# Kernel optimization log

Hardware: AMD Instinct MI355X
Metric: run time of the kernel (lower is better)

Reference implementation:

```python
import jax, jax.numpy as jnp
import numpy as np

N = 100000   # nodes
D = 128      # embedding dim
E = 1600000  # edges (avg in-degree 16)
EPS = 1e-15
MAX_TANH_ARG = 1.0 - 1e-7  # keep arctanh finite


def _logmap0(x):
    # Poincare-ball logmap at the origin: artanh(||x||) * x / ||x||
    norm = jnp.linalg.norm(x, axis=-1, keepdims=True)
    safe = jnp.maximum(norm, EPS)
    return jnp.arctanh(jnp.clip(norm, 0.0, MAX_TANH_ARG)) * x / safe


def _expmap0(v):
    # Poincare-ball expmap at the origin: tanh(||v||) * v / ||v||
    norm = jnp.linalg.norm(v, axis=-1, keepdims=True)
    safe = jnp.maximum(norm, EPS)
    return jnp.tanh(norm) * v / safe


def setup_inputs() -> dict:
    key = jax.random.key(0)
    k1, k2, k3, k4, k5 = jax.random.split(key, 5)
    # small norms keep points strictly inside the unit ball
    x = jax.random.normal(k1, (N, D), dtype=jnp.float32) * 0.01
    src = jax.random.randint(k2, (E,), 0, N)
    dst = jax.random.randint(k3, (E,), 0, N)
    W = jax.random.normal(k4, (D, D), dtype=jnp.float32) * (1.0 / np.sqrt(D))
    b = jax.random.normal(k5, (D,), dtype=jnp.float32) * 0.01
    return {"x": x, "W": W, "b": b, "src": src, "dst": dst}


def reference(x, W, b, src, dst):
    # logmap to tangent space at origin
    tangent_x = _logmap0(x)
    # linear layer (nn.Linear: x @ W^T + b)
    h = tangent_x @ W.T + b  # [N, D]
    # copy_u + mean aggregation over in-neighbors (DGL update_all)
    msg_sum = jax.ops.segment_sum(h[src], dst, num_segments=N)      # [N, D]
    deg = jax.ops.segment_sum(jnp.ones((E,), h.dtype), dst, num_segments=N)
    neigh = msg_sum / jnp.maximum(deg, 1.0)[:, None]  # zero-degree nodes -> 0 (DGL mean)
    # expmap back onto the Poincare ball
    return _expmap0(neigh)
```

## Files before the change

### kernel.cpp

```cpp
#include <hip/hip_runtime.h>
#include <hip/hip_fp16.h>
#include <math.h>

constexpr int D = 128;
constexpr int BSH = 9;
constexpr int BNODES = 1 << BSH;
constexpr int NBLK = 256;

typedef __attribute__((ext_vector_type(8))) short bf16x8;
typedef __attribute__((ext_vector_type(4))) float f32x4;

__device__ inline short f2bf(float f) {
    unsigned u = __builtin_bit_cast(unsigned, f);
    u = (u + 0x7FFFu + ((u >> 16) & 1u)) >> 16;
    return (short)u;
}

__global__ __launch_bounds__(256) void part_hist_kernel(
    const int* __restrict__ dst, int* __restrict__ blkhist,
    int nEdges, int NB)
{
    __shared__ int hist[256];
    int t = threadIdx.x;
    hist[t] = 0;
    __syncthreads();

    int per = (nEdges + gridDim.x - 1) / gridDim.x;
    int i0 = blockIdx.x * per;
    int i1 = min(nEdges, i0 + per);
    for (int i = i0 + t; i < i1; i += 256)
        atomicAdd(&hist[dst[i] >> BSH], 1);
    __syncthreads();
    if (t < NB) blkhist[t * NBLK + blockIdx.x] = hist[t];
}

__global__ __launch_bounds__(256) void part_scan1_kernel(
    int* __restrict__ blkhist, int* __restrict__ btot)
{
    __shared__ int s[256];
    int b = blockIdx.x;
    int t = threadIdx.x;
    int v = blkhist[b * NBLK + t];
    s[t] = v;
    __syncthreads();
    for (int off = 1; off < 256; off <<= 1) {
        int xv = (t >= off) ? s[t - off] : 0;
        __syncthreads();
        if (t >= off) s[t] += xv;
        __syncthreads();
    }
    blkhist[b * NBLK + t] = s[t] - v;
    if (t == 255) btot[b] = s[255];
}

__global__ __launch_bounds__(256) void part_scan2_kernel(
    const int* __restrict__ btot, int* __restrict__ bbase,
    int NB, int nEdges)
{
    __shared__ int s[256];
    int t = threadIdx.x;
    int v = (t < NB) ? btot[t] : 0;
    s[t] = v;
    __syncthreads();
    for (int off = 1; off < 256; off <<= 1) {
        int xv = (t >= off) ? s[t - off] : 0;
        __syncthreads();
        if (t >= off) s[t] += xv;
        __syncthreads();
    }
    if (t < NB) bbase[t] = s[t] - v;
    if (t == 0) bbase[NB] = nEdges;
}

__global__ __launch_bounds__(256) void part_scatter_kernel(
    const int* __restrict__ src, const int* __restrict__ dst,
    const int* __restrict__ blkhist, const int* __restrict__ bbase,
    unsigned* __restrict__ part, int nEdges, int NB)
{
    __shared__ int cur[256];
    int t = threadIdx.x;
    cur[t] = (t < NB) ? (blkhist[t * NBLK + blockIdx.x] + bbase[t]) : 0;
    __syncthreads();

    int per = (nEdges + gridDim.x - 1) / gridDim.x;
    int i0 = blockIdx.x * per;
    int i1 = min(nEdges, i0 + per);
    for (int i = i0 + t; i < i1; i += 256) {
        int d = dst[i];
        int b = d >> BSH;
        int p = atomicAdd(&cur[b], 1);
        part[p] = (unsigned)src[i] | ((unsigned)(d & (BNODES - 1)) << 17);
    }
}

__global__ __launch_bounds__(256) void bucket_csr_kernel(
    const unsigned* __restrict__ part, const int* __restrict__ bbase,
    int* __restrict__ rowptr, float* __restrict__ degf,
    int* __restrict__ csr_src, int nNodes, int NB, int nEdges)
{
    __shared__ int cnt[BNODES];
    __shared__ int excl[BNODES];
    __shared__ int cur[BNODES];
    __shared__ int s[256];

    int b = blockIdx.x;
    int t = threadIdx.x;
    int bb = bbase[b], be = bbase[b + 1];

    cnt[t] = 0; cnt[t + 256] = 0;
    cur[t] = 0; cur[t + 256] = 0;
    __syncthreads();

    for (int i = bb + t; i < be; i += 256)
        atomicAdd(&cnt[part[i] >> 17], 1);
    __syncthreads();

    int a0 = cnt[2 * t], a1 = cnt[2 * t + 1];
    s[t] = a0 + a1;
    __syncthreads();
    for (int off = 1; off < 256; off <<= 1) {
        int xv = (t >= off) ? s[t - off] : 0;
        __syncthreads();
        if (t >= off) s[t] += xv;
        __syncthreads();
    }
    int pbase = (t > 0) ? s[t - 1] : 0;
    excl[2 * t]     = pbase;
    excl[2 * t + 1] = pbase + a0;
    __syncthreads();

    int node0 = b << BSH;
#pragma unroll
    for (int q = 0; q < 2; ++q) {
        int j = t + q * 256;
        int d = node0 + j;
        if (d < nNodes) {
            rowptr[d] = bb + excl[j];
            degf[d]   = (float)cnt[j];
        }
    }
    if (b == NB - 1 && t == 0) rowptr[nNodes] = nEdges;

    for (int i = bb + t; i < be; i += 256) {
        unsigned v = part[i];
        int dloc = v >> 17;
        int p = bb + excl[dloc] + atomicAdd(&cur[dloc], 1);
        csr_src[p] = (int)(v & 0x1FFFFu);
    }
}

__global__ __launch_bounds__(256) void hist_win_kernel(
    const int* __restrict__ dst, int* __restrict__ count,
    int nEdges, int winSize)
{
    int pass    = blockIdx.x & 7;
    int slice   = blockIdx.x >> 3;
    int nSlices = gridDim.x >> 3;
    int lo = pass * winSize;
    int hi = lo + winSize;

    int stride = nSlices * blockDim.x;
    for (int i = slice * blockDim.x + threadIdx.x; i < nEdges; i += stride) {
        int d = dst[i];
        if (d >= lo && d < hi) atomicAdd(&count[d], 1);
    }
}

__global__ __launch_bounds__(256) void scan_block_kernel(
    const int* __restrict__ count, int* __restrict__ rowptr,
    int* __restrict__ blksums, int n)
{
    __shared__ int sums[256];
    int t = threadIdx.x;
    int base = blockIdx.x * 1024 + t * 4;
    int v[4];
    int s = 0;
#pragma unroll
    for (int j = 0; j < 4; ++j) { v[j] = (base + j < n) ? count[base + j] : 0; s += v[j]; }
    sums[t] = s;
    __syncthreads();
    for (int off = 1; off < 256; off <<= 1) {
        int xv = (t >= off) ? sums[t - off] : 0;
        __syncthreads();
        if (t >= off) sums[t] += xv;
        __syncthreads();
    }
    int run = (t > 0) ? sums[t - 1] : 0;
#pragma unroll
    for (int j = 0; j < 4; ++j) { if (base + j < n) rowptr[base + j] = run; run += v[j]; }
    if (t == 255) blksums[blockIdx.x] = sums[255];
}

__global__ __launch_bounds__(256) void scan_totals_kernel(
    int* __restrict__ blksums, int* __restrict__ rowptr,
    int numBlocks, int n, int E)
{
    __shared__ int s[256];
    int t = threadIdx.x;
    s[t] = (t < numBlocks) ? blksums[t] : 0;
    __syncthreads();
    for (int off = 1; off < 256; off <<= 1) {
        int xv = (t >= off) ? s[t - off] : 0;
        __syncthreads();
        if (t >= off) s[t] += xv;
        __syncthreads();
    }
    if (t < numBlocks) blksums[t] = (t > 0) ? s[t - 1] : 0;
    if (t == 0) rowptr[n] = E;
}

__global__ __launch_bounds__(256) void add_offsets_kernel(
    int* __restrict__ rowptr, const int* __restrict__ blksums, int n)
{
    int i = blockIdx.x * 256 + threadIdx.x;
    if (i < n) rowptr[i] += blksums[i >> 10];
}

__global__ __launch_bounds__(256) void fill_win_kernel(
    const int* __restrict__ src, const int* __restrict__ dst,
    const int* __restrict__ rowptr, int* __restrict__ count,
    int* __restrict__ csr_src, int nEdges, int winSize)
{
    int pass    = blockIdx.x & 7;
    int slice   = blockIdx.x >> 3;
    int nSlices = gridDim.x >> 3;
    int lo = pass * winSize;
    int hi = lo + winSize;

    int stride = nSlices * blockDim.x;
    for (int i = slice * blockDim.x + threadIdx.x; i < nEdges; i += stride) {
        int d = dst[i];
        if (d >= lo && d < hi) {
            int pos = rowptr[d] + atomicSub(&count[d], 1) - 1;
            csr_src[pos] = src[i];
        }
    }
}

__global__ __launch_bounds__(256) void deg_from_rowptr_kernel(
    const int* __restrict__ rowptr, float* __restrict__ degf, int n)
{
    int i = blockIdx.x * 256 + threadIdx.x;
    if (i < n) degf[i] = (float)(rowptr[i + 1] - rowptr[i]);
}

__global__ __launch_bounds__(256) void tangent_kernel(
    const float* __restrict__ x, __half* __restrict__ th, int nNodes)
{
    int n    = (blockIdx.x * 256 + threadIdx.x) >> 6;
    int lane = threadIdx.x & 63;
    if (n >= nNodes) return;
    float2 xv = *reinterpret_cast<const float2*>(x + (size_t)n * D + lane * 2);
    float ss = xv.x * xv.x + xv.y * xv.y;
    ss += __shfl_xor(ss, 1);
    ss += __shfl_xor(ss, 2);
    ss += __shfl_xor(ss, 4);
    ss += __shfl_xor(ss, 8);
    ss += __shfl_xor(ss, 16);
    ss += __shfl_xor(ss, 32);
    float norm = sqrtf(ss);
    float ncl  = fminf(norm, 1.0f - 1e-7f);
    float at   = 0.5f * logf((1.0f + ncl) / (1.0f - ncl));
    float sc   = at / fmaxf(norm, 1e-15f);
    __half2 h = __float22half2_rn(make_float2(xv.x * sc, xv.y * sc));
    *(reinterpret_cast<__half2*>(th + (size_t)n * D) + lane) = h;
}

__global__ __launch_bounds__(256) void scale_kernel(
    const float* __restrict__ x, float* __restrict__ scale, int nNodes)
{
    int node = (blockIdx.x * 256 + threadIdx.x) >> 6;
    int lane = threadIdx.x & 63;
    if (node >= nNodes) return;
    float2 xv = *reinterpret_cast<const float2*>(x + (size_t)node * D + lane * 2);
    float ss = xv.x * xv.x + xv.y * xv.y;
    ss += __shfl_xor(ss, 1);
    ss += __shfl_xor(ss, 2);
    ss += __shfl_xor(ss, 4);
    ss += __shfl_xor(ss, 8);
    ss += __shfl_xor(ss, 16);
    ss += __shfl_xor(ss, 32);
    if (lane == 0) {
        float norm = sqrtf(ss);
        float ncl  = fminf(norm, 1.0f - 1e-7f);
        float at   = 0.5f * logf((1.0f + ncl) / (1.0f - ncl));
        scale[node] = at / fmaxf(norm, 1e-15f);
    }
}

__global__ __launch_bounds__(256) void gather_h16b_kernel(
    const __half* __restrict__ th,
    const int* __restrict__ csr_src, const int* __restrict__ rowptr,
    short* __restrict__ msgb, int nNodes)
{
    int n    = blockIdx.x * 4 + (threadIdx.x >> 6);
    int lane = threadIdx.x & 63;
    if (n >= nNodes) return;
    int grp = lane >> 4;
    int sl  = lane & 15;

    int beg = rowptr[n];
    int cnt = rowptr[n + 1] - beg;

    __half2 z = __float2half2_rn(0.0f);
    __half2 acc0[4] = {z, z, z, z};
    __half2 acc1[4] = {z, z, z, z};

    int k = grp;
    for (; k + 12 < cnt; k += 16) {
        int s0 = csr_src[beg + k];
        int s1 = csr_src[beg + k + 4];
        int s2 = csr_src[beg + k + 8];
        int s3 = csr_src[beg + k + 12];
        float4 r0 = *reinterpret_cast<const float4*>(th + (size_t)s0 * D + sl * 8);
        float4 r1 = *reinterpret_cast<const float4*>(th + (size_t)s1 * D + sl * 8);
        float4 r2 = *reinterpret_cast<const float4*>(th + (size_t)s2 * D + sl * 8);
        float4 r3 = *reinterpret_cast<const float4*>(th + (size_t)s3 * D + sl * 8);
        const __half2* h0 = reinterpret_cast<const __half2*>(&r0);
        const __half2* h1 = reinterpret_cast<const __half2*>(&r1);
        const __half2* h2 = reinterpret_cast<const __half2*>(&r2);
        const __half2* h3 = reinterpret_cast<const __half2*>(&r3);
#pragma unroll
        for (int j = 0; j < 4; ++j) {
            acc0[j] = __hadd2(acc0[j], h0[j]);
            acc1[j] = __hadd2(acc1[j], h1[j]);
            acc0[j] = __hadd2(acc0[j], h2[j]);
            acc1[j] = __hadd2(acc1[j], h3[j]);
        }
    }
    for (; k < cnt; k += 4) {
        int s0 = csr_src[beg + k];
        float4 r0 = *reinterpret_cast<const float4*>(th + (size_t)s0 * D + sl * 8);
        const __half2* h0 = reinterpret_cast<const __half2*>(&r0);
#pragma unroll
        for (int j = 0; j < 4; ++j) acc0[j] = __hadd2(acc0[j], h0[j]);
    }
#pragma unroll
    for (int j = 0; j < 4; ++j) {
        acc0[j] = __hadd2(acc0[j], acc1[j]);
        float f16 = __shfl_xor(__builtin_bit_cast(float, acc0[j]), 16);
        acc0[j] = __hadd2(acc0[j], __builtin_bit_cast(__half2, f16));
        float f32v = __shfl_xor(__builtin_bit_cast(float, acc0[j]), 32);
        acc0[j] = __hadd2(acc0[j], __builtin_bit_cast(__half2, f32v));
    }
    if (grp == 0) {
        short s8[8];
#pragma unroll
        for (int j = 0; j < 4; ++j) {
            float2 f = __half22float2(acc0[j]);
            s8[2 * j]     = f2bf(f.x);
            s8[2 * j + 1] = f2bf(f.y);
        }
        *reinterpret_cast<float4*>(msgb + (size_t)n * D + sl * 8) =
            *reinterpret_cast<float4*>(s8);
    }
}

__global__ __launch_bounds__(256) void gather_h16_kernel(
    const __half* __restrict__ th,
    const int* __restrict__ csr_src, const int* __restrict__ rowptr,
    float* __restrict__ msg, int nNodes)
{
    int n    = blockIdx.x * 4 + (threadIdx.x >> 6);
    int lane = threadIdx.x & 63;
    if (n >= nNodes) return;
    int grp = lane >> 4;
    int sl  = lane & 15;

    int beg = rowptr[n];
    int cnt = rowptr[n + 1] - beg;

    __half2 z = __float2half2_rn(0.0f);
    __half2 acc0[4] = {z, z, z, z};
    __half2 acc1[4] = {z, z, z, z};

    int k = grp;
    for (; k + 12 < cnt; k += 16) {
        int s0 = csr_src[beg + k];
        int s1 = csr_src[beg + k + 4];
        int s2 = csr_src[beg + k + 8];
        int s3 = csr_src[beg + k + 12];
        float4 r0 = *reinterpret_cast<const float4*>(th + (size_t)s0 * D + sl * 8);
        float4 r1 = *reinterpret_cast<const float4*>(th + (size_t)s1 * D + sl * 8);
        float4 r2 = *reinterpret_cast<const float4*>(th + (size_t)s2 * D + sl * 8);
        float4 r3 = *reinterpret_cast<const float4*>(th + (size_t)s3 * D + sl * 8);
        const __half2* h0 = reinterpret_cast<const __half2*>(&r0);
        const __half2* h1 = reinterpret_cast<const __half2*>(&r1);
        const __half2* h2 = reinterpret_cast<const __half2*>(&r2);
        const __half2* h3 = reinterpret_cast<const __half2*>(&r3);
#pragma unroll
        for (int j = 0; j < 4; ++j) {
            acc0[j] = __hadd2(acc0[j], h0[j]);
            acc1[j] = __hadd2(acc1[j], h1[j]);
            acc0[j] = __hadd2(acc0[j], h2[j]);
            acc1[j] = __hadd2(acc1[j], h3[j]);
        }
    }
    for (; k < cnt; k += 4) {
        int s0 = csr_src[beg + k];
        float4 r0 = *reinterpret_cast<const float4*>(th + (size_t)s0 * D + sl * 8);
        const __half2* h0 = reinterpret_cast<const __half2*>(&r0);
#pragma unroll
        for (int j = 0; j < 4; ++j) acc0[j] = __hadd2(acc0[j], h0[j]);
    }
#pragma unroll
    for (int j = 0; j < 4; ++j) {
        acc0[j] = __hadd2(acc0[j], acc1[j]);
        float f16 = __shfl_xor(__builtin_bit_cast(float, acc0[j]), 16);
        acc0[j] = __hadd2(acc0[j], __builtin_bit_cast(__half2, f16));
        float f32v = __shfl_xor(__builtin_bit_cast(float, acc0[j]), 32);
        acc0[j] = __hadd2(acc0[j], __builtin_bit_cast(__half2, f32v));
    }
    if (grp == 0) {
        float2 f0 = __half22float2(acc0[0]);
        float2 f1 = __half22float2(acc0[1]);
        float2 f2 = __half22float2(acc0[2]);
        float2 f3 = __half22float2(acc0[3]);
        float4 o0 = make_float4(f0.x, f0.y, f1.x, f1.y);
        float4 o1 = make_float4(f2.x, f2.y, f3.x, f3.y);
        *reinterpret_cast<float4*>(msg + (size_t)n * D + sl * 8)     = o0;
        *reinterpret_cast<float4*>(msg + (size_t)n * D + sl * 8 + 4) = o1;
    }
}

__global__ __launch_bounds__(256) void gather_kernel(
    const float* __restrict__ x, const float* __restrict__ scale,
    const int* __restrict__ csr_src, const int* __restrict__ rowptr,
    float* __restrict__ msg, float* __restrict__ degf, int nNodes)
{
    int n    = blockIdx.x * 4 + (threadIdx.x >> 6);
    int lane = threadIdx.x & 63;
    if (n >= nNodes) return;

    int beg = rowptr[n], end = rowptr[n + 1];
    float2 acc0 = make_float2(0.0f, 0.0f);
    float2 acc1 = make_float2(0.0f, 0.0f);
    int e = beg;
    for (; e + 3 < end; e += 4) {
        int s0 = csr_src[e],     s1 = csr_src[e + 1];
        int s2 = csr_src[e + 2], s3 = csr_src[e + 3];
        float sc0 = scale[s0], sc1 = scale[s1];
        float sc2 = scale[s2], sc3 = scale[s3];
        float2 a = *reinterpret_cast<const float2*>(x + (size_t)s0 * D + lane * 2);
        float2 b = *reinterpret_cast<const float2*>(x + (size_t)s1 * D + lane * 2);
        float2 c = *reinterpret_cast<const float2*>(x + (size_t)s2 * D + lane * 2);
        float2 d = *reinterpret_cast<const float2*>(x + (size_t)s3 * D + lane * 2);
        acc0.x += sc0 * a.x;  acc0.y += sc0 * a.y;
        acc1.x += sc1 * b.x;  acc1.y += sc1 * b.y;
        acc0.x += sc2 * c.x;  acc0.y += sc2 * c.y;
        acc1.x += sc3 * d.x;  acc1.y += sc3 * d.y;
    }
    for (; e < end; ++e) {
        int s0 = csr_src[e];
        float sc0 = scale[s0];
        float2 a = *reinterpret_cast<const float2*>(x + (size_t)s0 * D + lane * 2);
        acc0.x += sc0 * a.x;  acc0.y += sc0 * a.y;
    }
    acc0.x += acc1.x;  acc0.y += acc1.y;
    *reinterpret_cast<float2*>(msg + (size_t)n * D + lane * 2) = acc0;
    if (lane == 0) degf[n] = (float)(end - beg);
}

__global__ __launch_bounds__(256) void edge_scatter_kernel(
    const float* __restrict__ x,
    const int* __restrict__ src,
    const int* __restrict__ dst,
    float* __restrict__ msg,
    float* __restrict__ deg,
    int nEdges)
{
    long long t = (long long)blockIdx.x * blockDim.x + threadIdx.x;
    int edge = (int)(t >> 5);
    int lane = (int)(t & 31);
    if (edge >= nEdges) return;

    int s = src[edge];
    int d = dst[edge];

    const float4 xv = *reinterpret_cast<const float4*>(x + (size_t)s * D + lane * 4);
    float ss = xv.x * xv.x + xv.y * xv.y + xv.z * xv.z + xv.w * xv.w;
    ss += __shfl_xor(ss, 1);
    ss += __shfl_xor(ss, 2);
    ss += __shfl_xor(ss, 4);
    ss += __shfl_xor(ss, 8);
    ss += __shfl_xor(ss, 16);

    float norm = sqrtf(ss);
    float ncl  = fminf(norm, 1.0f - 1e-7f);
    float at   = 0.5f * logf((1.0f + ncl) / (1.0f - ncl));
    float scale = at / fmaxf(norm, 1e-15f);

    float* mrow = msg + (size_t)d * D + lane * 4;
    unsafeAtomicAdd(mrow + 0, xv.x * scale);
    unsafeAtomicAdd(mrow + 1, xv.y * scale);
    unsafeAtomicAdd(mrow + 2, xv.z * scale);
    unsafeAtomicAdd(mrow + 3, xv.w * scale);
    if (lane == 0) unsafeAtomicAdd(deg + d, 1.0f);
}

__global__ __launch_bounds__(256) void gemm_mfma_b_kernel(
    const short* __restrict__ msgb, const float* __restrict__ deg,
    const float* __restrict__ W, const float* __restrict__ bias,
    float* __restrict__ out, int nNodes)
{
    __shared__ short sW[128][136];

    const int t = threadIdx.x;

#pragma unroll
    for (int p = 0; p < 16; ++p) {
        int chunk = p * 256 + t;
        int row = chunk >> 5;
        int c4  = (chunk & 31) * 4;
        float4 v = *reinterpret_cast<const float4*>(W + row * 128 + c4);
        short4 s;
        s.x = f2bf(v.x); s.y = f2bf(v.y); s.z = f2bf(v.z); s.w = f2bf(v.w);
        *reinterpret_cast<short4*>(&sW[row][c4]) = s;
    }
    __syncthreads();

    const int wave = t >> 6;
    const int lane = t & 63;
    const int l15  = lane & 15;
    const int lhi  = lane >> 4;
    const int m0   = blockIdx.x * 64 + wave * 16;

    int arow = m0 + l15;
    if (arow >= nNodes) arow = nNodes - 1;
    const short* ap = msgb + (size_t)arow * D + lhi * 8;
    bf16x8 a[4];
#pragma unroll
    for (int kc = 0; kc < 4; ++kc)
        a[kc] = *reinterpret_cast<const bf16x8*>(ap + kc * 32);

    f32x4 acc[8];
#pragma unroll
    for (int ct = 0; ct < 8; ++ct) acc[ct] = (f32x4){0.f, 0.f, 0.f, 0.f};

#pragma unroll
    for (int ct = 0; ct < 8; ++ct) {
#pragma unroll
        for (int kc = 0; kc < 4; ++kc) {
            bf16x8 bfrag = *reinterpret_cast<const bf16x8*>(
                &sW[ct * 16 + l15][kc * 32 + lhi * 8]);
            acc[ct] = __builtin_amdgcn_mfma_f32_16x16x32_bf16(a[kc], bfrag, acc[ct], 0, 0, 0);
        }
    }

    float bv[8];
#pragma unroll
    for (int ct = 0; ct < 8; ++ct) bv[ct] = bias[ct * 16 + l15];

#pragma unroll
    for (int r = 0; r < 4; ++r) {
        int row = m0 + lhi * 4 + r;
        int rc  = row < nNodes ? row : nNodes - 1;
        float dg  = deg[rc];
        float inv = 1.0f / fmaxf(dg, 1.0f);
        float v[8];
        float ss = 0.0f;
#pragma unroll
        for (int ct = 0; ct < 8; ++ct) {
            v[ct] = acc[ct][r] * inv + bv[ct];
            ss += v[ct] * v[ct];
        }
        ss += __shfl_xor(ss, 1);
        ss += __shfl_xor(ss, 2);
        ss += __shfl_xor(ss, 4);
        ss += __shfl_xor(ss, 8);
        float norm = sqrtf(ss);
        float sc = (dg > 0.0f) ? (tanhf(norm) / fmaxf(norm, 1e-15f)) : 0.0f;
        if (row < nNodes) {
#pragma unroll
            for (int ct = 0; ct < 8; ++ct)
                out[(size_t)row * D + ct * 16 + l15] = v[ct] * sc;
        }
    }
}

__global__ __launch_bounds__(256) void gemm_mfma_kernel(
    const float* msg, const float* __restrict__ deg,
    const float* __restrict__ W, const float* __restrict__ bias,
    float* out, int nNodes)
{
    __shared__ short sW[128][136];

    const int t = threadIdx.x;

#pragma unroll
    for (int p = 0; p < 16; ++p) {
        int chunk = p * 256 + t;
        int row = chunk >> 5;
        int c4  = (chunk & 31) * 4;
        float4 v = *reinterpret_cast<const float4*>(W + row * 128 + c4);
        short4 s;
        s.x = f2bf(v.x); s.y = f2bf(v.y); s.z = f2bf(v.z); s.w = f2bf(v.w);
        *reinterpret_cast<short4*>(&sW[row][c4]) = s;
    }
    __syncthreads();

    const int wave = t >> 6;
    const int lane = t & 63;
    const int l15  = lane & 15;
    const int lhi  = lane >> 4;
    const int m0   = blockIdx.x * 64 + wave * 16;

    int arow = m0 + l15;
    if (arow >= nNodes) arow = nNodes - 1;
    const float* ap = msg + (size_t)arow * D + lhi * 8;
    bf16x8 a[4];
#pragma unroll
    for (int kc = 0; kc < 4; ++kc) {
        float4 v0 = *reinterpret_cast<const float4*>(ap + kc * 32);
        float4 v1 = *reinterpret_cast<const float4*>(ap + kc * 32 + 4);
        bf16x8 f;
        f[0] = f2bf(v0.x); f[1] = f2bf(v0.y); f[2] = f2bf(v0.z); f[3] = f2bf(v0.w);
        f[4] = f2bf(v1.x); f[5] = f2bf(v1.y); f[6] = f2bf(v1.z); f[7] = f2bf(v1.w);
        a[kc] = f;
    }

    f32x4 acc[8];
#pragma unroll
    for (int ct = 0; ct < 8; ++ct) acc[ct] = (f32x4){0.f, 0.f, 0.f, 0.f};

#pragma unroll
    for (int ct = 0; ct < 8; ++ct) {
#pragma unroll
        for (int kc = 0; kc < 4; ++kc) {
            bf16x8 bfrag = *reinterpret_cast<const bf16x8*>(
                &sW[ct * 16 + l15][kc * 32 + lhi * 8]);
            acc[ct] = __builtin_amdgcn_mfma_f32_16x16x32_bf16(a[kc], bfrag, acc[ct], 0, 0, 0);
        }
    }

    float bv[8];
#pragma unroll
    for (int ct = 0; ct < 8; ++ct) bv[ct] = bias[ct * 16 + l15];

#pragma unroll
    for (int r = 0; r < 4; ++r) {
        int row = m0 + lhi * 4 + r;
        int rc  = row < nNodes ? row : nNodes - 1;
        float dg  = deg[rc];
        float inv = 1.0f / fmaxf(dg, 1.0f);
        float v[8];
        float ss = 0.0f;
#pragma unroll
        for (int ct = 0; ct < 8; ++ct) {
            v[ct] = acc[ct][r] * inv + bv[ct];
            ss += v[ct] * v[ct];
        }
        ss += __shfl_xor(ss, 1);
        ss += __shfl_xor(ss, 2);
        ss += __shfl_xor(ss, 4);
        ss += __shfl_xor(ss, 8);
        float norm = sqrtf(ss);
        float sc = (dg > 0.0f) ? (tanhf(norm) / fmaxf(norm, 1e-15f)) : 0.0f;
        if (row < nNodes) {
#pragma unroll
            for (int ct = 0; ct < 8; ++ct)
                out[(size_t)row * D + ct * 16 + l15] = v[ct] * sc;
        }
    }
}

static inline size_t align256(size_t o) { return (o + 255) & ~(size_t)255; }

extern "C" void kernel_launch(void* const* d_in, const int* in_sizes, int n_in,
                              void* d_out, int out_size, void* d_ws, size_t ws_size,
                              hipStream_t stream) {
    const float* x   = (const float*)d_in[0];
    const float* W   = (const float*)d_in[1];
    const float* b   = (const float*)d_in[2];
    const int*   src = (const int*)d_in[3];
    const int*   dst = (const int*)d_in[4];
    float* out = (float*)d_out;

    int nNodes = in_sizes[0] / D;
    int nEdges = in_sizes[3];
    int NB = (nNodes + BNODES - 1) >> BSH;

    char* ws = (char*)d_ws;
    size_t off = 0;
    float* degf    = (float*)(ws + off); off = align256(off + sizeof(float) * nNodes);
    int*   count   = (int*)  (ws + off); off = align256(off + sizeof(int) * nNodes);
    int*   rowptr  = (int*)  (ws + off); off = align256(off + sizeof(int) * (nNodes + 1));
    float* scl     = (float*)(ws + off); off = align256(off + sizeof(float) * nNodes);
    int*   blksums = (int*)  (ws + off); off = align256(off + sizeof(int) * 256);
    int*   bbase   = (int*)  (ws + off); off = align256(off + sizeof(int) * 257);
    int*   btot    = (int*)  (ws + off); off = align256(off + sizeof(int) * 256);
    int*   blkhist = (int*)  (ws + off); off = align256(off + sizeof(int) * NBLK * 256);
    int*   csr_src = (int*)  (ws + off); off = align256(off + sizeof(int) * nEdges);
    size_t need_mid = off;
    unsigned* part = (unsigned*)(ws + off);
    __half*   th   = (__half*)  (ws + off);
    size_t szA = sizeof(__half) * (size_t)nNodes * D;
    if (sizeof(unsigned) * (size_t)nEdges > szA) szA = sizeof(unsigned) * (size_t)nEdges;
    off = align256(off + szA);
    size_t need_part = off;
    short* msgb = (short*)(ws + off); off = align256(off + sizeof(short) * (size_t)nNodes * D);
    size_t need_msgb = off;

    float* msg = out;

    int numScanBlocks = (nNodes + 1023) / 1024;
    bool part_ok = (ws_size >= need_part) && (nNodes <= 131072) && (NB <= 256);
    bool bf16msg = part_ok && (ws_size >= need_msgb);
    bool mid_ok  = (ws_size >= need_mid) && (numScanBlocks <= 256);

    if (part_ok) {
        part_hist_kernel<<<NBLK, 256, 0, stream>>>(dst, blkhist, nEdges, NB);
        part_scan1_kernel<<<NB, 256, 0, stream>>>(blkhist, btot);
        part_scan2_kernel<<<1, 256, 0, stream>>>(btot, bbase, NB, nEdges);
        part_scatter_kernel<<<NBLK, 256, 0, stream>>>(src, dst, blkhist, bbase, part, nEdges, NB);
        bucket_csr_kernel<<<NB, 256, 0, stream>>>(part, bbase, rowptr, degf,
                                                  csr_src, nNodes, NB, nEdges);
        tangent_kernel<<<(nNodes + 3) / 4, 256, 0, stream>>>(x, th, nNodes);
        if (bf16msg) {
            gather_h16b_kernel<<<(nNodes + 3) / 4, 256, 0, stream>>>(th, csr_src, rowptr, msgb, nNodes);
            gemm_mfma_b_kernel<<<(nNodes + 63) / 64, 256, 0, stream>>>(msgb, degf, W, b, out, nNodes);
        } else {
            gather_h16_kernel<<<(nNodes + 3) / 4, 256, 0, stream>>>(th, csr_src, rowptr, msg, nNodes);
            gemm_mfma_kernel<<<(nNodes + 63) / 64, 256, 0, stream>>>(msg, degf, W, b, out, nNodes);
        }
        return;
    }

    if (mid_ok) {
        hipMemsetAsync(count, 0, sizeof(int) * nNodes, stream);
        int winSize = (nNodes + 7) / 8;
        hist_win_kernel<<<4096, 256, 0, stream>>>(dst, count, nEdges, winSize);
        scan_block_kernel<<<numScanBlocks, 256, 0, stream>>>(count, rowptr, blksums, nNodes);
        scan_totals_kernel<<<1, 256, 0, stream>>>(blksums, rowptr, numScanBlocks, nNodes, nEdges);
        add_offsets_kernel<<<(nNodes + 255) / 256, 256, 0, stream>>>(rowptr, blksums, nNodes);
        fill_win_kernel<<<4096, 256, 0, stream>>>(src, dst, rowptr, count, csr_src, nEdges, winSize);
        deg_from_rowptr_kernel<<<(nNodes + 255) / 256, 256, 0, stream>>>(rowptr, degf, nNodes);

        scale_kernel<<<(nNodes + 3) / 4, 256, 0, stream>>>(x, scl, nNodes);
        gather_kernel<<<(nNodes + 3) / 4, 256, 0, stream>>>(x, scl, csr_src, rowptr, msg, degf, nNodes);
        gemm_mfma_kernel<<<(nNodes + 63) / 64, 256, 0, stream>>>(msg, degf, W, b, out, nNodes);
        return;
    }

    {
        float* deg = (float*)d_ws;
        hipMemsetAsync(msg, 0, (size_t)nNodes * D * sizeof(float), stream);
        hipMemsetAsync(deg, 0, (size_t)nNodes * sizeof(float), stream);
        long long threads = (long long)nEdges * 32;
        int blocks = (int)((threads + 255) / 256);
        edge_scatter_kernel<<<blocks, 256, 0, stream>>>(x, src, dst, msg, (float*)d_ws, nEdges);
        gemm_mfma_kernel<<<(nNodes + 63) / 64, 256, 0, stream>>>(msg, (float*)d_ws, W, b, out, nNodes);
    }
}
```

Before: 149.5 us.

## Fuse tangent map into histogram launch, drop scan2 kernel, gather two nodes per wave

Result: faster. 140.7 us (median of 2 runs) (-5.9%).

```diff
diff --git a/kernel.cpp b/kernel.cpp
--- a/kernel.cpp
+++ b/kernel.cpp
@@ -16,239 +16,30 @@
     return (short)u;
 }
 
-__global__ __launch_bounds__(256) void part_hist_kernel(
+__global__ __launch_bounds__(256) void hist_tangent_kernel(
     const int* __restrict__ dst, int* __restrict__ blkhist,
-    int nEdges, int NB)
+    int nEdges, int NB,
+    const float* __restrict__ x, __half* __restrict__ th, int nNodes)
 {
     __shared__ int hist[256];
     int t = threadIdx.x;
-    hist[t] = 0;
-    __syncthreads();
-
-    int per = (nEdges + gridDim.x - 1) / gridDim.x;
-    int i0 = blockIdx.x * per;
-    int i1 = min(nEdges, i0 + per);
-    for (int i = i0 + t; i < i1; i += 256)
-        atomicAdd(&hist[dst[i] >> BSH], 1);
-    __syncthreads();
-    if (t < NB) blkhist[t * NBLK + blockIdx.x] = hist[t];
-}
-
-__global__ __launch_bounds__(256) void part_scan1_kernel(
-    int* __restrict__ blkhist, int* __restrict__ btot)
-{
-    __shared__ int s[256];
-    int b = blockIdx.x;
-    int t = threadIdx.x;
-    int v = blkhist[b * NBLK + t];
-    s[t] = v;
-    __syncthreads();
-    for (int off = 1; off < 256; off <<= 1) {
-        int xv = (t >= off) ? s[t - off] : 0;
-        __syncthreads();
-        if (t >= off) s[t] += xv;
-        __syncthreads();
-    }
-    blkhist[b * NBLK + t] = s[t] - v;
-    if (t == 255) btot[b] = s[255];
-}
-
-__global__ __launch_bounds__(256) void part_scan2_kernel(
-    const int* __restrict__ btot, int* __restrict__ bbase,
-    int NB, int nEdges)
-{
-    __shared__ int s[256];
-    int t = threadIdx.x;
-    int v = (t < NB) ? btot[t] : 0;
-    s[t] = v;
-    __syncthreads();
-    for (int off = 1; off < 256; off <<= 1) {
-        int xv = (t >= off) ? s[t - off] : 0;
-        __syncthreads();
-        if (t >= off) s[t] += xv;
-        __syncthreads();
-    }
-    if (t < NB) bbase[t] = s[t] - v;
-    if (t == 0) bbase[NB] = nEdges;
-}
-
-__global__ __launch_bounds__(256) void part_scatter_kernel(
-    const int* __restrict__ src, const int* __restrict__ dst,
-    const int* __restrict__ blkhist, const int* __restrict__ bbase,
-    unsigned* __restrict__ part, int nEdges, int NB)
-{
-    __shared__ int cur[256];
-    int t = threadIdx.x;
-    cur[t] = (t < NB) ? (blkhist[t * NBLK + blockIdx.x] + bbase[t]) : 0;
-    __syncthreads();
-
-    int per = (nEdges + gridDim.x - 1) / gridDim.x;
-    int i0 = blockIdx.x * per;
-    int i1 = min(nEdges, i0 + per);
-    for (int i = i0 + t; i < i1; i += 256) {
-        int d = dst[i];
-        int b = d >> BSH;
-        int p = atomicAdd(&cur[b], 1);
-        part[p] = (unsigned)src[i] | ((unsigned)(d & (BNODES - 1)) << 17);
-    }
-}
-
-__global__ __launch_bounds__(256) void bucket_csr_kernel(
-    const unsigned* __restrict__ part, const int* __restrict__ bbase,
-    int* __restrict__ rowptr, float* __restrict__ degf,
-    int* __restrict__ csr_src, int nNodes, int NB, int nEdges)
-{
-    __shared__ int cnt[BNODES];
-    __shared__ int excl[BNODES];
-    __shared__ int cur[BNODES];
-    __shared__ int s[256];
-
-    int b = blockIdx.x;
-    int t = threadIdx.x;
-    int bb = bbase[b], be = bbase[b + 1];
-
-    cnt[t] = 0; cnt[t + 256] = 0;
-    cur[t] = 0; cur[t + 256] = 0;
-    __syncthreads();
-
-    for (int i = bb + t; i < be; i += 256)
-        atomicAdd(&cnt[part[i] >> 17], 1);
-    __syncthreads();
-
-    int a0 = cnt[2 * t], a1 = cnt[2 * t + 1];
-    s[t] = a0 + a1;
-    __syncthreads();
-    for (int off = 1; off < 256; off <<= 1) {
-        int xv = (t >= off) ? s[t - off] : 0;
-        __syncthreads();
-        if (t >= off) s[t] += xv;
-        __syncthreads();
-    }
-    int pbase = (t > 0) ? s[t - 1] : 0;
-    excl[2 * t]     = pbase;
-    excl[2 * t + 1] = pbase + a0;
-    __syncthreads();
-
-    int node0 = b << BSH;
-#pragma unroll
-    for (int q = 0; q < 2; ++q) {
-        int j = t + q * 256;
-        int d = node0 + j;
-        if (d < nNodes) {
-            rowptr[d] = bb + excl[j];
-            degf[d]   = (float)cnt[j];
-        }
-    }
-    if (b == NB - 1 && t == 0) rowptr[nNodes] = nEdges;
-
-    for (int i = bb + t; i < be; i += 256) {
-        unsigned v = part[i];
-        int dloc = v >> 17;
-        int p = bb + excl[dloc] + atomicAdd(&cur[dloc], 1);
-        csr_src[p] = (int)(v & 0x1FFFFu);
-    }
-}
-
-__global__ __launch_bounds__(256) void hist_win_kernel(
-    const int* __restrict__ dst, int* __restrict__ count,
-    int nEdges, int winSize)
-{
-    int pass    = blockIdx.x & 7;
-    int slice   = blockIdx.x >> 3;
-    int nSlices = gridDim.x >> 3;
-    int lo = pass * winSize;
-    int hi = lo + winSize;
-
-    int stride = nSlices * blockDim.x;
-    for (int i = slice * blockDim.x + threadIdx.x; i < nEdges; i += stride) {
-        int d = dst[i];
-        if (d >= lo && d < hi) atomicAdd(&count[d], 1);
-    }
-}
-
-__global__ __launch_bounds__(256) void scan_block_kernel(
-    const int* __restrict__ count, int* __restrict__ rowptr,
-    int* __restrict__ blksums, int n)
-{
-    __shared__ int sums[256];
-    int t = threadIdx.x;
-    int base = blockIdx.x * 1024 + t * 4;
-    int v[4];
-    int s = 0;
-#pragma unroll
-    for (int j = 0; j < 4; ++j) { v[j] = (base + j < n) ? count[base + j] : 0; s += v[j]; }
-    sums[t] = s;
-    __syncthreads();
-    for (int off = 1; off < 256; off <<= 1) {
-        int xv = (t >= off) ? sums[t - off] : 0;
-        __syncthreads();
-        if (t >= off) sums[t] += xv;
-        __syncthreads();
-    }
-    int run = (t > 0) ? sums[t - 1] : 0;
-#pragma unroll
-    for (int j = 0; j < 4; ++j) { if (base + j < n) rowptr[base + j] = run; run += v[j]; }
-    if (t == 255) blksums[blockIdx.x] = sums[255];
-}
-
-__global__ __launch_bounds__(256) void scan_totals_kernel(
-    int* __restrict__ blksums, int* __restrict__ rowptr,
-    int numBlocks, int n, int E)
-{
-    __shared__ int s[256];
-    int t = threadIdx.x;
-    s[t] = (t < numBlocks) ? blksums[t] : 0;
-    __syncthreads();
-    for (int off = 1; off < 256; off <<= 1) {
-        int xv = (t >= off) ? s[t - off] : 0;
-        __syncthreads();
-        if (t >= off) s[t] += xv;
-        __syncthreads();
-    }
-    if (t < numBlocks) blksums[t] = (t > 0) ? s[t - 1] : 0;
-    if (t == 0) rowptr[n] = E;
-}
-
-__global__ __launch_bounds__(256) void add_offsets_kernel(
-    int* __restrict__ rowptr, const int* __restrict__ blksums, int n)
-{
-    int i = blockIdx.x * 256 + threadIdx.x;
-    if (i < n) rowptr[i] += blksums[i >> 10];
-}
-
-__global__ __launch_bounds__(256) void fill_win_kernel(
-    const int* __restrict__ src, const int* __restrict__ dst,
-    const int* __restrict__ rowptr, int* __restrict__ count,
-    int* __restrict__ csr_src, int nEdges, int winSize)
-{
-    int pass    = blockIdx.x & 7;
-    int slice   = blockIdx.x >> 3;
-    int nSlices = gridDim.x >> 3;
-    int lo = pass * winSize;
-    int hi = lo + winSize;
-
-    int stride = nSlices * blockDim.x;
-    for (int i = slice * blockDim.x + threadIdx.x; i < nEdges; i += stride) {
-        int d = dst[i];
-        if (d >= lo && d < hi) {
-            int pos = rowptr[d] + atomicSub(&count[d], 1) - 1;
-            csr_src[pos] = src[i];
-        }
-    }
-}
-
-__global__ __launch_bounds__(256) void deg_from_rowptr_kernel(
-    const int* __restrict__ rowptr, float* __restrict__ degf, int n)
-{
-    int i = blockIdx.x * 256 + threadIdx.x;
-    if (i < n) degf[i] = (float)(rowptr[i + 1] - rowptr[i]);
-}
-
-__global__ __launch_bounds__(256) void tangent_kernel(
-    const float* __restrict__ x, __half* __restrict__ th, int nNodes)
-{
-    int n    = (blockIdx.x * 256 + threadIdx.x) >> 6;
-    int lane = threadIdx.x & 63;
+
+    if (blockIdx.x < NBLK) {
+        hist[t] = 0;
+        __syncthreads();
+        int per = (nEdges + NBLK - 1) / NBLK;
+        int i0 = blockIdx.x * per;
+        int i1 = min(nEdges, i0 + per);
+        for (int i = i0 + t; i < i1; i += 256)
+            atomicAdd(&hist[dst[i] >> BSH], 1);
+        __syncthreads();
+        if (t < NB) blkhist[t * NBLK + blockIdx.x] = hist[t];
+        return;
+    }
+
+    int nb = blockIdx.x - NBLK;
+    int n    = (nb * 256 + t) >> 6;
+    int lane = t & 63;
     if (n >= nNodes) return;
     float2 xv = *reinterpret_cast<const float2*>(x + (size_t)n * D + lane * 2);
     float ss = xv.x * xv.x + xv.y * xv.y;
@@ -264,6 +55,221 @@
     float sc   = at / fmaxf(norm, 1e-15f);
     __half2 h = __float22half2_rn(make_float2(xv.x * sc, xv.y * sc));
     *(reinterpret_cast<__half2*>(th + (size_t)n * D) + lane) = h;
+}
+
+__global__ __launch_bounds__(256) void part_scan1_kernel(
+    int* __restrict__ blkhist, int* __restrict__ btot)
+{
+    __shared__ int s[256];
+    int b = blockIdx.x;
+    int t = threadIdx.x;
+    int v = blkhist[b * NBLK + t];
+    s[t] = v;
+    __syncthreads();
+    for (int off = 1; off < 256; off <<= 1) {
+        int xv = (t >= off) ? s[t - off] : 0;
+        __syncthreads();
+        if (t >= off) s[t] += xv;
+        __syncthreads();
+    }
+    blkhist[b * NBLK + t] = s[t] - v;
+    if (t == 255) btot[b] = s[255];
+}
+
+__global__ __launch_bounds__(256) void part_scatter_kernel(
+    const int* __restrict__ src, const int* __restrict__ dst,
+    const int* __restrict__ blkhist, const int* __restrict__ btot,
+    unsigned* __restrict__ part, int nEdges, int NB)
+{
+    __shared__ int sb[256];
+    __shared__ int cur[256];
+    int t = threadIdx.x;
+    int v = (t < NB) ? btot[t] : 0;
+    sb[t] = v;
+    __syncthreads();
+    for (int off = 1; off < 256; off <<= 1) {
+        int xv = (t >= off) ? sb[t - off] : 0;
+        __syncthreads();
+        if (t >= off) sb[t] += xv;
+        __syncthreads();
+    }
+    int bbase_t = sb[t] - v;
+    cur[t] = (t < NB) ? (blkhist[t * NBLK + blockIdx.x] + bbase_t) : 0;
+    __syncthreads();
+
+    int per = (nEdges + gridDim.x - 1) / gridDim.x;
+    int i0 = blockIdx.x * per;
+    int i1 = min(nEdges, i0 + per);
+    for (int i = i0 + t; i < i1; i += 256) {
+        int d = dst[i];
+        int b = d >> BSH;
+        int p = atomicAdd(&cur[b], 1);
+        part[p] = (unsigned)src[i] | ((unsigned)(d & (BNODES - 1)) << 17);
+    }
+}
+
+__global__ __launch_bounds__(256) void bucket_csr_kernel(
+    const unsigned* __restrict__ part, const int* __restrict__ btot,
+    int* __restrict__ rowptr, float* __restrict__ degf,
+    int* __restrict__ csr_src, int nNodes, int NB, int nEdges)
+{
+    __shared__ int cnt[BNODES];
+    __shared__ int excl[BNODES];
+    __shared__ int cur[BNODES];
+    __shared__ int s[256];
+    __shared__ int sBB[2];
+
+    int b = blockIdx.x;
+    int t = threadIdx.x;
+
+    int v = (t < NB) ? btot[t] : 0;
+    s[t] = v;
+    __syncthreads();
+    for (int off = 1; off < 256; off <<= 1) {
+        int xv = (t >= off) ? s[t - off] : 0;
+        __syncthreads();
+        if (t >= off) s[t] += xv;
+        __syncthreads();
+    }
+    if (t == b) { sBB[0] = s[t] - v; sBB[1] = s[t]; }
+    __syncthreads();
+    int bb = sBB[0], be = sBB[1];
+
+    cnt[t] = 0; cnt[t + 256] = 0;
+    cur[t] = 0; cur[t + 256] = 0;
+    __syncthreads();
+
+    for (int i = bb + t; i < be; i += 256)
+        atomicAdd(&cnt[part[i] >> 17], 1);
+    __syncthreads();
+
+    int a0 = cnt[2 * t], a1 = cnt[2 * t + 1];
+    s[t] = a0 + a1;
+    __syncthreads();
+    for (int off = 1; off < 256; off <<= 1) {
+        int xv = (t >= off) ? s[t - off] : 0;
+        __syncthreads();
+        if (t >= off) s[t] += xv;
+        __syncthreads();
+    }
+    int pbase = (t > 0) ? s[t - 1] : 0;
+    excl[2 * t]     = pbase;
+    excl[2 * t + 1] = pbase + a0;
+    __syncthreads();
+
+    int node0 = b << BSH;
+#pragma unroll
+    for (int q = 0; q < 2; ++q) {
+        int j = t + q * 256;
+        int d = node0 + j;
+        if (d < nNodes) {
+            rowptr[d] = bb + excl[j];
+            degf[d]   = (float)cnt[j];
+        }
+    }
+    if (b == NB - 1 && t == 0) rowptr[nNodes] = nEdges;
+
+    for (int i = bb + t; i < be; i += 256) {
+        unsigned vv = part[i];
+        int dloc = vv >> 17;
+        int p = bb + excl[dloc] + atomicAdd(&cur[dloc], 1);
+        csr_src[p] = (int)(vv & 0x1FFFFu);
+    }
+}
+
+__global__ __launch_bounds__(256) void hist_win_kernel(
+    const int* __restrict__ dst, int* __restrict__ count,
+    int nEdges, int winSize)
+{
+    int pass    = blockIdx.x & 7;
+    int slice   = blockIdx.x >> 3;
+    int nSlices = gridDim.x >> 3;
+    int lo = pass * winSize;
+    int hi = lo + winSize;
+
+    int stride = nSlices * blockDim.x;
+    for (int i = slice * blockDim.x + threadIdx.x; i < nEdges; i += stride) {
+        int d = dst[i];
+        if (d >= lo && d < hi) atomicAdd(&count[d], 1);
+    }
+}
+
+__global__ __launch_bounds__(256) void scan_block_kernel(
+    const int* __restrict__ count, int* __restrict__ rowptr,
+    int* __restrict__ blksums, int n)
+{
+    __shared__ int sums[256];
+    int t = threadIdx.x;
+    int base = blockIdx.x * 1024 + t * 4;
+    int v[4];
+    int s = 0;
+#pragma unroll
+    for (int j = 0; j < 4; ++j) { v[j] = (base + j < n) ? count[base + j] : 0; s += v[j]; }
+    sums[t] = s;
+    __syncthreads();
+    for (int off = 1; off < 256; off <<= 1) {
+        int xv = (t >= off) ? sums[t - off] : 0;
+        __syncthreads();
+        if (t >= off) sums[t] += xv;
+        __syncthreads();
+    }
+    int run = (t > 0) ? sums[t - 1] : 0;
+#pragma unroll
+    for (int j = 0; j < 4; ++j) { if (base + j < n) rowptr[base + j] = run; run += v[j]; }
+    if (t == 255) blksums[blockIdx.x] = sums[255];
+}
+
+__global__ __launch_bounds__(256) void scan_totals_kernel(
+    int* __restrict__ blksums, int* __restrict__ rowptr,
+    int numBlocks, int n, int E)
+{
+    __shared__ int s[256];
+    int t = threadIdx.x;
+    s[t] = (t < numBlocks) ? blksums[t] : 0;
+    __syncthreads();
+    for (int off = 1; off < 256; off <<= 1) {
+        int xv = (t >= off) ? s[t - off] : 0;
+        __syncthreads();
+        if (t >= off) s[t] += xv;
+        __syncthreads();
+    }
+    if (t < numBlocks) blksums[t] = (t > 0) ? s[t - 1] : 0;
+    if (t == 0) rowptr[n] = E;
+}
+
+__global__ __launch_bounds__(256) void add_offsets_kernel(
+    int* __restrict__ rowptr, const int* __restrict__ blksums, int n)
+{
+    int i = blockIdx.x * 256 + threadIdx.x;
+    if (i < n) rowptr[i] += blksums[i >> 10];
+}
+
+__global__ __launch_bounds__(256) void fill_win_kernel(
+    const int* __restrict__ src, const int* __restrict__ dst,
+    const int* __restrict__ rowptr, int* __restrict__ count,
+    int* __restrict__ csr_src, int nEdges, int winSize)
+{
+    int pass    = blockIdx.x & 7;
+    int slice   = blockIdx.x >> 3;
+    int nSlices = gridDim.x >> 3;
+    int lo = pass * winSize;
+    int hi = lo + winSize;
+
+    int stride = nSlices * blockDim.x;
+    for (int i = slice * blockDim.x + threadIdx.x; i < nEdges; i += stride) {
+        int d = dst[i];
+        if (d >= lo && d < hi) {
+            int pos = rowptr[d] + atomicSub(&count[d], 1) - 1;
+            csr_src[pos] = src[i];
+        }
+    }
+}
+
+__global__ __launch_bounds__(256) void deg_from_rowptr_kernel(
+    const int* __restrict__ rowptr, float* __restrict__ degf, int n)
+{
+    int i = blockIdx.x * 256 + threadIdx.x;
+    if (i < n) degf[i] = (float)(rowptr[i + 1] - rowptr[i]);
 }
 
 __global__ __launch_bounds__(256) void scale_kernel(
@@ -288,30 +294,34 @@
     }
 }
 
-__global__ __launch_bounds__(256) void gather_h16b_kernel(
+__global__ __launch_bounds__(256) void gather2_h16b_kernel(
     const __half* __restrict__ th,
     const int* __restrict__ csr_src, const int* __restrict__ rowptr,
     short* __restrict__ msgb, int nNodes)
 {
-    int n    = blockIdx.x * 4 + (threadIdx.x >> 6);
-    int lane = threadIdx.x & 63;
-    if (n >= nNodes) return;
-    int grp = lane >> 4;
-    int sl  = lane & 15;
-
-    int beg = rowptr[n];
-    int cnt = rowptr[n + 1] - beg;
+    int t    = threadIdx.x;
+    int lane = t & 63;
+    int wave = t >> 6;
+    int grp  = lane >> 4;
+    int np   = grp >> 1;
+    int g2   = grp & 1;
+    int sl   = lane & 15;
+
+    int n  = blockIdx.x * 8 + wave * 2 + np;
+    int nn = n < nNodes ? n : nNodes - 1;
+    int beg = rowptr[nn];
+    int cnt = rowptr[nn + 1] - beg;
 
     __half2 z = __float2half2_rn(0.0f);
     __half2 acc0[4] = {z, z, z, z};
     __half2 acc1[4] = {z, z, z, z};
 
-    int k = grp;
-    for (; k + 12 < cnt; k += 16) {
+    int k = g2;
+    for (; k + 6 < cnt; k += 8) {
         int s0 = csr_src[beg + k];
-        int s1 = csr_src[beg + k + 4];
-        int s2 = csr_src[beg + k + 8];
-        int s3 = csr_src[beg + k + 12];
+        int s1 = csr_src[beg + k + 2];
+        int s2 = csr_src[beg + k + 4];
+        int s3 = csr_src[beg + k + 6];
         float4 r0 = *reinterpret_cast<const float4*>(th + (size_t)s0 * D + sl * 8);
         float4 r1 = *reinterpret_cast<const float4*>(th + (size_t)s1 * D + sl * 8);
         float4 r2 = *reinterpret_cast<const float4*>(th + (size_t)s2 * D + sl * 8);
@@ -328,7 +338,7 @@
             acc1[j] = __hadd2(acc1[j], h3[j]);
         }
     }
-    for (; k < cnt; k += 4) {
+    for (; k < cnt; k += 2) {
         int s0 = csr_src[beg + k];
         float4 r0 = *reinterpret_cast<const float4*>(th + (size_t)s0 * D + sl * 8);
         const __half2* h0 = reinterpret_cast<const __half2*>(&r0);
@@ -338,12 +348,10 @@
 #pragma unroll
     for (int j = 0; j < 4; ++j) {
         acc0[j] = __hadd2(acc0[j], acc1[j]);
-        float f16 = __shfl_xor(__builtin_bit_cast(float, acc0[j]), 16);
-        acc0[j] = __hadd2(acc0[j], __builtin_bit_cast(__half2, f16));
-        float f32v = __shfl_xor(__builtin_bit_cast(float, acc0[j]), 32);
-        acc0[j] = __hadd2(acc0[j], __builtin_bit_cast(__half2, f32v));
-    }
-    if (grp == 0) {
+        float fx = __shfl_xor(__builtin_bit_cast(float, acc0[j]), 16);
+        acc0[j] = __hadd2(acc0[j], __builtin_bit_cast(__half2, fx));
+    }
+    if (g2 == 0 && n < nNodes) {
         short s8[8];
 #pragma unroll
         for (int j = 0; j < 4; ++j) {
@@ -687,37 +695,42 @@
     int*   rowptr  = (int*)  (ws + off); off = align256(off + sizeof(int) * (nNodes + 1));
     float* scl     = (float*)(ws + off); off = align256(off + sizeof(float) * nNodes);
     int*   blksums = (int*)  (ws + off); off = align256(off + sizeof(int) * 256);
-    int*   bbase   = (int*)  (ws + off); off = align256(off + sizeof(int) * 257);
     int*   btot    = (int*)  (ws + off); off = align256(off + sizeof(int) * 256);
     int*   blkhist = (int*)  (ws + off); off = align256(off + sizeof(int) * NBLK * 256);
     int*   csr_src = (int*)  (ws + off); off = align256(off + sizeof(int) * nEdges);
     size_t need_mid = off;
+
+    size_t part_sz = sizeof(unsigned) * (size_t)nEdges;
+    size_t msgb_sz = sizeof(short) * (size_t)nNodes * D;
+    size_t th_sz   = sizeof(__half) * (size_t)nNodes * D;
+
     unsigned* part = (unsigned*)(ws + off);
-    __half*   th   = (__half*)  (ws + off);
-    size_t szA = sizeof(__half) * (size_t)nNodes * D;
-    if (sizeof(unsigned) * (size_t)nEdges > szA) szA = sizeof(unsigned) * (size_t)nEdges;
-    off = align256(off + szA);
-    size_t need_part = off;
-    short* msgb = (short*)(ws + off); off = align256(off + sizeof(short) * (size_t)nNodes * D);
-    size_t need_msgb = off;
+    short*    msgb = (short*)   (ws + off);
+    size_t off_lo = align256(off + part_sz);
+    size_t off_hi = align256(off + (part_sz > msgb_sz ? part_sz : msgb_sz));
+    __half* th_lo = (__half*)(ws + off_lo);
+    __half* th_hi = (__half*)(ws + off_hi);
+    size_t need_lo = align256(off_lo + th_sz);
+    size_t need_hi = align256(off_hi + th_sz);
 
     float* msg = out;
 
     int numScanBlocks = (nNodes + 1023) / 1024;
-    bool part_ok = (ws_size >= need_part) && (nNodes <= 131072) && (NB <= 256);
-    bool bf16msg = part_ok && (ws_size >= need_msgb);
+    bool part_ok = (ws_size >= need_lo) && (nNodes <= 131072) && (NB <= 256);
+    bool bf16msg = (ws_size >= need_hi) && (nNodes <= 131072) && (NB <= 256);
     bool mid_ok  = (ws_size >= need_mid) && (numScanBlocks <= 256);
 
-    if (part_ok) {
-        part_hist_kernel<<<NBLK, 256, 0, stream>>>(dst, blkhist, nEdges, NB);
+    if (part_ok || bf16msg) {
+        __half* th = bf16msg ? th_hi : th_lo;
+        int TB = (nNodes + 3) / 4;
+        hist_tangent_kernel<<<NBLK + TB, 256, 0, stream>>>(
+            dst, blkhist, nEdges, NB, x, th, nNodes);
         part_scan1_kernel<<<NB, 256, 0, stream>>>(blkhist, btot);
-        part_scan2_kernel<<<1, 256, 0, stream>>>(btot, bbase, NB, nEdges);
-        part_scatter_kernel<<<NBLK, 256, 0, stream>>>(src, dst, blkhist, bbase, part, nEdges, NB);
-        bucket_csr_kernel<<<NB, 256, 0, stream>>>(part, bbase, rowptr, degf,
+        part_scatter_kernel<<<NBLK, 256, 0, stream>>>(src, dst, blkhist, btot, part, nEdges, NB);
+        bucket_csr_kernel<<<NB, 256, 0, stream>>>(part, btot, rowptr, degf,
                                                   csr_src, nNodes, NB, nEdges);
-        tangent_kernel<<<(nNodes + 3) / 4, 256, 0, stream>>>(x, th, nNodes);
         if (bf16msg) {
-            gather_h16b_kernel<<<(nNodes + 3) / 4, 256, 0, stream>>>(th, csr_src, rowptr, msgb, nNodes);
+            gather2_h16b_kernel<<<(nNodes + 7) / 8, 256, 0, stream>>>(th, csr_src, rowptr, msgb, nNodes);
             gemm_mfma_b_kernel<<<(nNodes + 63) / 64, 256, 0, stream>>>(msgb, degf, W, b, out, nNodes);
         } else {
             gather_h16_kernel<<<(nNodes + 3) / 4, 256, 0, stream>>>(th, csr_src, rowptr, msg, nNodes);
```
